# Optimization experiments

Hardware: AMD Instinct MI355X
Metric: run time of the kernel (lower is better)

## Reference

```python
import jax, jax.numpy as jnp
import numpy as np

E = 262144   # num edges
T = 1048576  # num triplets
H = 128      # hidden_channels
IE = 64      # int_emb_size
NR = 6       # num_radial
NS = 7       # num_spherical
BD = 8       # basis_emb_size_dist
BA = 8       # basis_emb_size_angle


def setup_inputs() -> dict:
    key = jax.random.key(0)
    ks = jax.random.split(key, 32)
    def rnd(k, shape, s=0.1):
        return jax.random.normal(k, shape, dtype=jnp.float32) * s
    return {
        "x1": rnd(ks[0], (T, H), 1.0),
        "x_old": rnd(ks[1], (E, H), 1.0),
        "rbf0": rnd(ks[2], (E, NR), 1.0),
        "sbf": rnd(ks[3], (T, NS * NR), 1.0),
        "idx_kj": jax.random.randint(ks[4], (T,), 0, E),
        "idx_ji": jax.random.randint(ks[5], (T,), 0, E),
        "W_rbf1": rnd(ks[6], (NR, BD)),
        "W_rbf2": rnd(ks[7], (BD, H)),
        "W_sbf1": rnd(ks[8], (NS * NR, BA)),
        "W_sbf2": rnd(ks[9], (BA, IE)),
        "W_rbf": rnd(ks[10], (NR, H)),
        "W_kj": rnd(ks[11], (H, H)), "b_kj": rnd(ks[12], (H,)),
        "W_ji": rnd(ks[13], (H, H)), "b_ji": rnd(ks[14], (H,)),
        "W_connect": rnd(ks[15], (H, H)), "b_connect": rnd(ks[16], (H,)),
        "W_get_up": rnd(ks[17], (H, H)), "b_get_up": rnd(ks[18], (H,)),
        "W_down": rnd(ks[19], (H, IE)), "b_down": rnd(ks[20], (IE,)),
        "W_up": rnd(ks[21], (IE, H)), "b_up": rnd(ks[22], (H,)),
        "res_before_W": rnd(ks[23], (1, 2, H, H)), "res_before_b": rnd(ks[24], (1, 2, H)),
        "W_lin": rnd(ks[25], (H, H)), "b_lin": rnd(ks[26], (H,)),
        "res_after_W": rnd(ks[27], (2, 2, H, H)), "res_after_b": rnd(ks[28], (2, 2, H)),
    }


def _residual(x, W, b):
    # x + act(lin2(act(lin1(x))))
    h = jax.nn.silu(x @ W[0] + b[0])
    return x + jax.nn.silu(h @ W[1] + b[1])


def reference(x1, x_old, rbf0, sbf, idx_kj, idx_ji, W_rbf1, W_rbf2, W_sbf1, W_sbf2,
              W_rbf, W_kj, b_kj, W_ji, b_ji, W_connect, b_connect, W_get_up, b_get_up,
              W_down, b_down, W_up, b_up, res_before_W, res_before_b, W_lin, b_lin,
              res_after_W, res_after_b):
    act = jax.nn.silu  # swish
    nE = x_old.shape[0]
    # aggregate plane features onto edges
    x_up = jax.ops.segment_sum(x1, idx_ji, num_segments=nE)
    x_up = act(x_up @ W_get_up + b_get_up)
    x_ji = act(x_old @ W_ji + b_ji)
    x_kj = act(x_old @ W_kj + b_kj)
    rbf = (rbf0 @ W_rbf1) @ W_rbf2            # [E, H]
    x_kj = x_kj * rbf
    x_kj = act(x_kj @ W_down + b_down)        # [E, IE]
    sbf_p = (sbf @ W_sbf1) @ W_sbf2           # [T, IE]
    x_kj = x_kj[idx_kj] * sbf_p               # gather edges -> triplets
    x_kj = jax.ops.segment_sum(x_kj, idx_ji, num_segments=nE)  # scatter back to edges
    x_kj = act(x_kj @ W_up + b_up)
    e1 = x_ji + x_kj
    e1 = act(e1 @ W_connect + b_connect) + x_up
    for i in range(res_before_W.shape[0]):
        e1 = _residual(e1, res_before_W[i], res_before_b[i])
    e1 = act(e1 @ W_lin + b_lin) + x_old
    for i in range(res_after_W.shape[0]):
        e1 = _residual(e1, res_after_W[i], res_after_b[i])
    e2 = (rbf0 @ W_rbf) * e1
    return (e1, e2)
```

## Files before the change

### kernel.cpp

```cpp
#include <hip/hip_runtime.h>

#define E_N 262144
#define T_N 1048576

typedef short  bf16x8  __attribute__((ext_vector_type(8)));
typedef short  bf16x4v __attribute__((ext_vector_type(4)));
typedef float  f32x4   __attribute__((ext_vector_type(4)));

#define OFF_KJ    0
#define OFF_DOWN  16384
#define OFF_UP    24576
#define OFF_JI    32768
#define OFF_GU    49152
#define OFF_CN    65536
#define OFF_RB0   81920
#define OFF_RB1   98304
#define OFF_LIN   114688
#define OFF_RA00  131072
#define OFF_RA01  147456
#define OFF_RA10  163840
#define OFF_RA11  180224
#define OFF_END   196608
#define WREG_BYTES 524288u

#define OFFB_AGG   0u
#define OFFB_XKJ   33554432u
#define OFFB_WREG  67108864u
#define OFFB_CNT   67633152u
#define OFFB_POS   68683776u
#define OFFB_TRI   69732352u
#define OFFB_BS    73926656u
#define OFFB_BP    73927680u

__device__ __forceinline__ float silu_f(float x) { return x / (1.0f + __expf(-x)); }

__device__ __forceinline__ unsigned short f2bf(float f) {
  union { float f; unsigned int u; } v; v.f = f;
  unsigned int u = v.u;
  return (unsigned short)((u + 0x7fffu + ((u >> 16) & 1u)) >> 16);
}
__device__ __forceinline__ float bf2f(unsigned short h) {
  union { unsigned int u; float f; } v; v.u = ((unsigned int)h) << 16;
  return v.f;
}

__device__ __forceinline__ unsigned cvtpk(float lo, float hi) {
  unsigned r;
  asm("v_cvt_pk_bf16_f32 %0, %1, %2" : "=v"(r) : "v"(lo), "v"(hi));
  return r;
}

template<int NC, int NR, int NTH>
__device__ __forceinline__ void stage_tile(const float* __restrict__ g, char* __restrict__ lds) {
  constexpr int RB = NC * 2;
  constexpr int C4 = NC / 4;
  for (int i = threadIdx.x; i < NR * C4; i += NTH) {
    int r = i / C4, c4 = i % C4;
    float4 v = *(const float4*)(g + (size_t)r * NC + c4 * 4);
    bf16x4v h;
    h[0] = (short)f2bf(v.x); h[1] = (short)f2bf(v.y);
    h[2] = (short)f2bf(v.z); h[3] = (short)f2bf(v.w);
    *(bf16x4v*)(lds + r * RB + ((c4 * 8) ^ ((r & 7) << 4))) = h;
  }
}

__device__ __forceinline__ void stage_tile_bf16_64(const unsigned short* __restrict__ g,
                                                   char* __restrict__ lds) {
  int i = threadIdx.x;
  int r = i >> 3, c = i & 7;
  int4 v = *(const int4*)((const char*)g + r * 128 + c * 16);
  *(int4*)(lds + r * 128 + ((c * 16) ^ ((r & 7) << 4))) = v;
}

template<int MREP, int NREP, int KSTEPS, int RB>
__device__ __forceinline__ void mfma_gemm(const char* __restrict__ lds, int row0, int col0,
                                          const unsigned short* __restrict__ WT, int lane,
                                          f32x4 (&acc)[MREP][NREP]) {
  const int kg = lane >> 4, r15 = lane & 15;
#pragma unroll
  for (int m = 0; m < MREP; ++m)
#pragma unroll
    for (int n = 0; n < NREP; ++n) acc[m][n] = (f32x4){0.f, 0.f, 0.f, 0.f};
#pragma unroll
  for (int kk = 0; kk < KSTEPS; ++kk) {
    bf16x8 a[MREP], bfr[NREP];
#pragma unroll
    for (int m = 0; m < MREP; ++m) {
      int row = row0 + m * 16 + r15;
      a[m] = *(const bf16x8*)(lds + row * RB + ((kk * 64 + kg * 16) ^ ((row & 7) << 4)));
    }
#pragma unroll
    for (int n = 0; n < NREP; ++n) {
      int nc = col0 + n * 16 + r15;
      bfr[n] = *(const bf16x8*)((const short*)WT + nc * (KSTEPS * 32) + kk * 32 + kg * 8);
    }
#pragma unroll
    for (int m = 0; m < MREP; ++m)
#pragma unroll
      for (int n = 0; n < NREP; ++n)
        acc[m][n] = __builtin_amdgcn_mfma_f32_16x16x32_bf16(a[m], bfr[n], acc[m][n], 0, 0, 0);
  }
}

template<int RB>
__device__ __forceinline__ void write_cd(char* __restrict__ lds, int wrow, int wcol, int lane,
                                         const f32x4 (&v)[2][2]) {
  const int kg = lane >> 4, r15 = lane & 15;
#pragma unroll
  for (int m = 0; m < 2; ++m)
#pragma unroll
    for (int n = 0; n < 2; ++n) {
      int col2 = (wcol + n * 16 + r15) * 2;
      int row0 = wrow + m * 16 + kg * 4;
      unsigned u0 = cvtpk(v[m][n][0], v[m][n][1]);
      unsigned u1 = cvtpk(v[m][n][2], v[m][n][3]);
      *(unsigned short*)(lds + (row0 + 0) * RB + (col2 ^ (((row0 + 0) & 7) << 4))) = (unsigned short)u0;
      *(unsigned short*)(lds + (row0 + 1) * RB + (col2 ^ (((row0 + 1) & 7) << 4))) = (unsigned short)(u0 >> 16);
      *(unsigned short*)(lds + (row0 + 2) * RB + (col2 ^ (((row0 + 2) & 7) << 4))) = (unsigned short)u1;
      *(unsigned short*)(lds + (row0 + 3) * RB + (col2 ^ (((row0 + 3) & 7) << 4))) = (unsigned short)(u1 >> 16);
    }
}

__global__ void __launch_bounds__(256) k_prep(
    const float* __restrict__ W_kj, const float* __restrict__ W_down,
    const float* __restrict__ W_up, const float* __restrict__ W_ji,
    const float* __restrict__ W_get_up, const float* __restrict__ W_connect,
    const float* __restrict__ rbW, const float* __restrict__ W_lin,
    const float* __restrict__ raW,
    const float* __restrict__ W_rbf1, const float* __restrict__ W_rbf2,
    unsigned short* __restrict__ wreg) {
  int b = blockIdx.x;
  if (b == 13) {
    float* W12 = (float*)(wreg + OFF_END);
    for (int i = threadIdx.x; i < 768; i += 256) {
      int r = i >> 7, n = i & 127;
      float s = 0.f;
#pragma unroll
      for (int q = 0; q < 8; ++q) s += W_rbf1[r * 8 + q] * W_rbf2[q * 128 + n];
      W12[i] = s;
    }
    return;
  }
  const float* src; int K = 128, N = 128; int off;
  switch (b) {
    case 0:  src = W_kj;          off = OFF_KJ;  break;
    case 1:  src = W_down;        off = OFF_DOWN; N = 64;  break;
    case 2:  src = W_up;          off = OFF_UP;   K = 64;  break;
    case 3:  src = W_ji;          off = OFF_JI;  break;
    case 4:  src = W_get_up;      off = OFF_GU;  break;
    case 5:  src = W_connect;     off = OFF_CN;  break;
    case 6:  src = rbW;           off = OFF_RB0; break;
    case 7:  src = rbW + 16384;   off = OFF_RB1; break;
    case 8:  src = W_lin;         off = OFF_LIN; break;
    case 9:  src = raW;           off = OFF_RA00; break;
    case 10: src = raW + 16384;   off = OFF_RA01; break;
    case 11: src = raW + 32768;   off = OFF_RA10; break;
    default: src = raW + 49152;   off = OFF_RA11; break;
  }
  unsigned short* dst = wreg + off;
  for (int i = threadIdx.x; i < K * N; i += 256) {
    int k = i / N, n = i % N;
    dst[n * K + k] = f2bf(src[i]);
  }
}

__global__ void __launch_bounds__(256) k_hist(const int* __restrict__ idx_ji,
                                              int* __restrict__ counts) {
  int t = blockIdx.x * 256 + threadIdx.x;
  atomicAdd(&counts[idx_ji[t]], 1);
}

__global__ void __launch_bounds__(1024) k_scan1(const int* __restrict__ counts,
                                                int* __restrict__ locpre,
                                                int* __restrict__ bsum) {
  __shared__ int s[1024];
  int i = blockIdx.x * 1024 + threadIdx.x;
  int v = counts[i];
  s[threadIdx.x] = v; __syncthreads();
  for (int o = 1; o < 1024; o <<= 1) {
    int t = (threadIdx.x >= o) ? s[threadIdx.x - o] : 0;
    __syncthreads();
    s[threadIdx.x] += t;
    __syncthreads();
  }
  locpre[i] = s[threadIdx.x] - v;
  if (threadIdx.x == 1023) bsum[blockIdx.x] = s[1023];
}

__global__ void __launch_bounds__(256) k_scan2(const int* __restrict__ bsum,
                                               int* __restrict__ bpre, int* __restrict__ offs) {
  __shared__ int s[256];
  int v = bsum[threadIdx.x];
  s[threadIdx.x] = v; __syncthreads();
  for (int o = 1; o < 256; o <<= 1) {
    int t = (threadIdx.x >= o) ? s[threadIdx.x - o] : 0;
    __syncthreads();
    s[threadIdx.x] += t;
    __syncthreads();
  }
  bpre[threadIdx.x] = s[threadIdx.x] - v;
  if (threadIdx.x == 0) offs[E_N] = T_N;
}

__global__ void __launch_bounds__(1024) k_scan3(const int* __restrict__ locpre,
                                                const int* __restrict__ bpre,
                                                int* __restrict__ offs,
                                                int* __restrict__ pos) {
  int i = blockIdx.x * 1024 + threadIdx.x;
  int v = locpre[i] + bpre[blockIdx.x];
  offs[i] = v;
  pos[i] = v;
}

__global__ void __launch_bounds__(256) k_fill(const int* __restrict__ idx_ji,
                                              int* __restrict__ pos, int* __restrict__ tri) {
  int t = blockIdx.x * 256 + threadIdx.x;
  int e = idx_ji[t];
  int slot = atomicAdd(&pos[e], 1);
  tri[slot] = t;
}

__global__ void __launch_bounds__(256) k_sbfp(const float* __restrict__ sbf,
                                              const float* __restrict__ W_sbf1,
                                              const float* __restrict__ W_sbf2,
                                              unsigned int* __restrict__ sbfp) {
  __shared__ float s_s[8][42];
  __shared__ float s_t8[8][8];
  int t0 = blockIdx.x * 8;
  for (int i = threadIdx.x; i < 8 * 42; i += 256)
    s_s[i / 42][i % 42] = sbf[(size_t)t0 * 42 + i];
  __syncthreads();
  if (threadIdx.x < 64) {
    int w8 = threadIdx.x >> 3, bb = threadIdx.x & 7;
    float s = 0.f;
#pragma unroll
    for (int r = 0; r < 42; ++r) s += s_s[w8][r] * W_sbf1[r * 8 + bb];
    s_t8[w8][bb] = s;
  }
  __syncthreads();
  int w8 = threadIdx.x >> 5, jj = threadIdx.x & 31;
  float sp0 = 0.f, sp1 = 0.f;
#pragma unroll
  for (int bb = 0; bb < 8; ++bb) {
    float tv = s_t8[w8][bb];
    sp0 += tv * W_sbf2[bb * 64 + jj * 2];
    sp1 += tv * W_sbf2[bb * 64 + jj * 2 + 1];
  }
  unsigned int u = (unsigned int)f2bf(sp0) | ((unsigned int)f2bf(sp1) << 16);
  sbfp[(size_t)(t0 + w8) * 32 + jj] = u;
}

__global__ void __launch_bounds__(256) k_aggB(const int* __restrict__ offs,
                                              const int* __restrict__ tri,
                                              const int* __restrict__ idx_kj,
                                              const unsigned int* __restrict__ sbfp,
                                              const unsigned int* __restrict__ xkj,
                                              unsigned int* __restrict__ agg) {
  int sub = threadIdx.x >> 5, jj = threadIdx.x & 31;
  int e = blockIdx.x * 8 + sub;
  int o0 = offs[e], o1 = offs[e + 1];
  float a0 = 0.f, a1 = 0.f;
  for (int i = o0; i < o1; ++i) {
    int t = tri[i];
    int kj = idx_kj[t];
    unsigned int sv = sbfp[(size_t)t * 32 + jj];
    unsigned int xv = xkj[(size_t)kj * 32 + jj];
    a0 += bf2f((unsigned short)(sv & 0xffff)) * bf2f((unsigned short)(xv & 0xffff));
    a1 += bf2f((unsigned short)(sv >> 16)) * bf2f((unsigned short)(xv >> 16));
  }
  agg[(size_t)e * 32 + jj] = (unsigned int)f2bf(a0) | ((unsigned int)f2bf(a1) << 16);
}

__global__ void __launch_bounds__(256) k_xupg(const int* __restrict__ offs,
                                              const int* __restrict__ tri,
                                              const float* __restrict__ x1,
                                              float* __restrict__ out) {
  int sub = threadIdx.x >> 6, h2 = threadIdx.x & 63;
  int e = blockIdx.x * 4 + sub;
  int o0 = offs[e], o1 = offs[e + 1];
  float a0 = 0.f, a1 = 0.f;
  for (int i = o0; i < o1; ++i) {
    int t = tri[i];
    float2 v = *(const float2*)(x1 + (size_t)t * 128 + h2 * 2);
    a0 += v.x; a1 += v.y;
  }
  *(float2*)(out + (size_t)e * 128 + h2 * 2) = make_float2(a0, a1);
}

__global__ void __launch_bounds__(512, 4) phaseA(
    const float* __restrict__ x_old, const float* __restrict__ rbf0,
    const unsigned short* __restrict__ wreg,
    const float* __restrict__ b_kj, const float* __restrict__ b_down,
    unsigned short* __restrict__ xkjdown) {
  __shared__ char lds[32768];
  char* B0 = lds;
  char* B1 = lds + 16384;
  const int tid = threadIdx.x, lane = tid & 63, wave = tid >> 6;
  const int kg = lane >> 4, r15 = lane & 15;
  const int wrow = (wave >> 2) * 32, wcol = (wave & 3) * 32;
  const size_t e_base = (size_t)blockIdx.x * 64;
  const float* W12 = (const float*)(wreg + OFF_END);

  stage_tile<128, 64, 512>(x_old + e_base * 128, B0);
  __syncthreads();

  f32x4 acc[2][2], val[2][2];
  mfma_gemm<2, 2, 4, 256>(B0, wrow, wcol, wreg + OFF_KJ, lane, acc);
#pragma unroll
  for (int n = 0; n < 2; ++n) {
    int col = wcol + n * 16 + r15;
    float bk = b_kj[col];
    float wc[6];
#pragma unroll
    for (int q = 0; q < 6; ++q) wc[q] = W12[q * 128 + col];
#pragma unroll
    for (int m = 0; m < 2; ++m)
#pragma unroll
      for (int r = 0; r < 4; ++r) {
        int row = wrow + m * 16 + kg * 4 + r;
        const float* rp = rbf0 + (e_base + row) * 6;
        float rv = rp[0]*wc[0] + rp[1]*wc[1] + rp[2]*wc[2] + rp[3]*wc[3] + rp[4]*wc[4] + rp[5]*wc[5];
        val[m][n][r] = silu_f(acc[m][n][r] + bk) * rv;
      }
  }
  write_cd<256>(B1, wrow, wcol, lane, val);
  __syncthreads();

  const int wrow2 = (wave >> 1) * 16, wcol2 = (wave & 1) * 32;
  f32x4 a2[1][2];
  mfma_gemm<1, 2, 4, 256>(B1, wrow2, wcol2, wreg + OFF_DOWN, lane, a2);
#pragma unroll
  for (int n = 0; n < 2; ++n) {
    int col = wcol2 + n * 16 + r15;
    float bd = b_down[col];
#pragma unroll
    for (int r = 0; r < 4; ++r) {
      int row = wrow2 + kg * 4 + r;
      xkjdown[(e_base + row) * 64 + col] = f2bf(silu_f(a2[0][n][r] + bd));
    }
  }
}

__global__ void __launch_bounds__(512, 4) phaseC1(
    const float* __restrict__ x_old, float* __restrict__ e1buf,
    const unsigned short* __restrict__ agg, const unsigned short* __restrict__ wreg,
    const float* __restrict__ b_up, const float* __restrict__ b_ji,
    const float* __restrict__ b_get_up, const float* __restrict__ b_connect,
    const float* __restrict__ rbB, const float* __restrict__ b_lin,
    const float* __restrict__ raB,
    const float* __restrict__ rbf0, const float* __restrict__ W_rbf,
    float* __restrict__ e2o) {
  __shared__ char lds[73728];
  char* X0   = lds;
  char* X1   = lds + 16384;
  char* X2   = lds + 32768;
  char* XOLD = lds + 49152;
  char* AGGB = lds + 65536;
  const int tid = threadIdx.x, lane = tid & 63, wave = tid >> 6;
  const int kg = lane >> 4, r15 = lane & 15;
  const int wrow = (wave >> 2) * 32, wcol = (wave & 3) * 32;
  const size_t e_base = (size_t)blockIdx.x * 64;

  stage_tile<128, 64, 512>(x_old + e_base * 128, XOLD);
  stage_tile<128, 64, 512>(e1buf + e_base * 128, X1);
  stage_tile_bf16_64(agg + e_base * 64, AGGB);
  __syncthreads();

  f32x4 acc[2][2], keep[2][2], h[2][2];

  mfma_gemm<2, 2, 2, 128>(AGGB, wrow, wcol, wreg + OFF_UP, lane, acc);
#pragma unroll
  for (int n = 0; n < 2; ++n) {
    float bu = b_up[wcol + n * 16 + r15];
#pragma unroll
    for (int m = 0; m < 2; ++m)
#pragma unroll
      for (int r = 0; r < 4; ++r) h[m][n][r] = silu_f(acc[m][n][r] + bu);
  }
  mfma_gemm<2, 2, 4, 256>(XOLD, wrow, wcol, wreg + OFF_JI, lane, acc);
#pragma unroll
  for (int n = 0; n < 2; ++n) {
    float bj = b_ji[wcol + n * 16 + r15];
#pragma unroll
    for (int m = 0; m < 2; ++m)
#pragma unroll
      for (int r = 0; r < 4; ++r) keep[m][n][r] = silu_f(acc[m][n][r] + bj) + h[m][n][r];
  }
  write_cd<256>(X0, wrow, wcol, lane, keep);
  __syncthreads();

  mfma_gemm<2, 2, 4, 256>(X1, wrow, wcol, wreg + OFF_GU, lane, acc);
#pragma unroll
  for (int n = 0; n < 2; ++n) {
    float bg = b_get_up[wcol + n * 16 + r15];
#pragma unroll
    for (int m = 0; m < 2; ++m)
#pragma unroll
      for (int r = 0; r < 4; ++r) h[m][n][r] = silu_f(acc[m][n][r] + bg);
  }
  mfma_gemm<2, 2, 4, 256>(X0, wrow, wcol, wreg + OFF_CN, lane, acc);
#pragma unroll
  for (int n = 0; n < 2; ++n) {
    float bc = b_connect[wcol + n * 16 + r15];
#pragma unroll
    for (int m = 0; m < 2; ++m)
#pragma unroll
      for (int r = 0; r < 4; ++r) keep[m][n][r] = silu_f(acc[m][n][r] + bc) + h[m][n][r];
  }
  write_cd<256>(X2, wrow, wcol, lane, keep);
  __syncthreads();

  mfma_gemm<2, 2, 4, 256>(X2, wrow, wcol, wreg + OFF_RB0, lane, acc);
#pragma unroll
  for (int n = 0; n < 2; ++n) {
    float bv = rbB[wcol + n * 16 + r15];
#pragma unroll
    for (int m = 0; m < 2; ++m)
#pragma unroll
      for (int r = 0; r < 4; ++r) h[m][n][r] = silu_f(acc[m][n][r] + bv);
  }
  write_cd<256>(X0, wrow, wcol, lane, h);
  __syncthreads();

  mfma_gemm<2, 2, 4, 256>(X0, wrow, wcol, wreg + OFF_RB1, lane, acc);
#pragma unroll
  for (int n = 0; n < 2; ++n) {
    float bv = rbB[128 + wcol + n * 16 + r15];
#pragma unroll
    for (int m = 0; m < 2; ++m)
#pragma unroll
      for (int r = 0; r < 4; ++r) keep[m][n][r] += silu_f(acc[m][n][r] + bv);
  }
  write_cd<256>(X1, wrow, wcol, lane, keep);
  __syncthreads();

  mfma_gemm<2, 2, 4, 256>(X1, wrow, wcol, wreg + OFF_LIN, lane, acc);
#pragma unroll
  for (int n = 0; n < 2; ++n) {
    int col = wcol + n * 16 + r15;
    float bl = b_lin[col];
#pragma unroll
    for (int m = 0; m < 2; ++m)
#pragma unroll
      for (int r = 0; r < 4; ++r) {
        int row = wrow + m * 16 + kg * 4 + r;
        float xo = bf2f(*(const unsigned short*)(XOLD + row * 256 + ((col * 2) ^ ((row & 7) << 4))));
        keep[m][n][r] = silu_f(acc[m][n][r] + bl) + xo;
      }
  }
  write_cd<256>(X2, wrow, wcol, lane, keep);
  __syncthreads();

  mfma_gemm<2, 2, 4, 256>(X2, wrow, wcol, wreg + OFF_RA00, lane, acc);
#pragma unroll
  for (int n = 0; n < 2; ++n) {
    float bv = raB[wcol + n * 16 + r15];
#pragma unroll
    for (int m = 0; m < 2; ++m)
#pragma unroll
      for (int r = 0; r < 4; ++r) h[m][n][r] = silu_f(acc[m][n][r] + bv);
  }
  write_cd<256>(X0, wrow, wcol, lane, h);
  __syncthreads();

  mfma_gemm<2, 2, 4, 256>(X0, wrow, wcol, wreg + OFF_RA01, lane, acc);
#pragma unroll
  for (int n = 0; n < 2; ++n) {
    float bv = raB[128 + wcol + n * 16 + r15];
#pragma unroll
    for (int m = 0; m < 2; ++m)
#pragma unroll
      for (int r = 0; r < 4; ++r) keep[m][n][r] += silu_f(acc[m][n][r] + bv);
  }
  write_cd<256>(X1, wrow, wcol, lane, keep);
  __syncthreads();

  mfma_gemm<2, 2, 4, 256>(X1, wrow, wcol, wreg + OFF_RA10, lane, acc);
#pragma unroll
  for (int n = 0; n < 2; ++n) {
    float bv = raB[256 + wcol + n * 16 + r15];
#pragma unroll
    for (int m = 0; m < 2; ++m)
#pragma unroll
      for (int r = 0; r < 4; ++r) h[m][n][r] = silu_f(acc[m][n][r] + bv);
  }
  write_cd<256>(X2, wrow, wcol, lane, h);
  __syncthreads();

  mfma_gemm<2, 2, 4, 256>(X2, wrow, wcol, wreg + OFF_RA11, lane, acc);
#pragma unroll
  for (int n = 0; n < 2; ++n) {
    int col = wcol + n * 16 + r15;
    float bv = raB[384 + col];
    float wc[6];
#pragma unroll
    for (int q = 0; q < 6; ++q) wc[q] = W_rbf[q * 128 + col];
#pragma unroll
    for (int m = 0; m < 2; ++m)
#pragma unroll
      for (int r = 0; r < 4; ++r) {
        int row = wrow + m * 16 + kg * 4 + r;
        size_t e = e_base + row;
        float val = keep[m][n][r] + silu_f(acc[m][n][r] + bv);
        e1buf[e * 128 + col] = val;
        if (e2o) {
          const float* rp = rbf0 + e * 6;
          float rv = rp[0]*wc[0] + rp[1]*wc[1] + rp[2]*wc[2] + rp[3]*wc[3] + rp[4]*wc[4] + rp[5]*wc[5];
          e2o[e * 128 + col] = val * rv;
        }
      }
  }
}

__global__ void __launch_bounds__(256) k_e2(const float* __restrict__ e1,
                                            const float* __restrict__ rbf0,
                                            const float* __restrict__ W_rbf,
                                            float* __restrict__ e2) {
  size_t gid = (size_t)blockIdx.x * 256 + threadIdx.x;
  int e = (int)(gid >> 5);
  int c = (int)(gid & 31) << 2;
  float r6[6];
#pragma unroll
  for (int r = 0; r < 6; ++r) r6[r] = rbf0[(size_t)e * 6 + r];
  float4 v = *(const float4*)(e1 + (size_t)e * 128 + c);
  float4 o;
  float rv;
  rv = 0.f;
#pragma unroll
  for (int r = 0; r < 6; ++r) rv += r6[r] * W_rbf[r * 128 + c + 0];
  o.x = v.x * rv;
  rv = 0.f;
#pragma unroll
  for (int r = 0; r < 6; ++r) rv += r6[r] * W_rbf[r * 128 + c + 1];
  o.y = v.y * rv;
  rv = 0.f;
#pragma unroll
  for (int r = 0; r < 6; ++r) rv += r6[r] * W_rbf[r * 128 + c + 2];
  o.z = v.z * rv;
  rv = 0.f;
#pragma unroll
  for (int r = 0; r < 6; ++r) rv += r6[r] * W_rbf[r * 128 + c + 3];
  o.w = v.w * rv;
  *(float4*)(e2 + (size_t)e * 128 + c) = o;
}

extern "C" void kernel_launch(void* const* d_in, const int* in_sizes, int n_in,
                              void* d_out, int out_size, void* d_ws, size_t ws_size,
                              hipStream_t stream) {
  const float* x1        = (const float*)d_in[0];
  const float* x_old     = (const float*)d_in[1];
  const float* rbf0      = (const float*)d_in[2];
  const float* sbf       = (const float*)d_in[3];
  const int*   idx_kj    = (const int*)d_in[4];
  const int*   idx_ji    = (const int*)d_in[5];
  const float* W_rbf1    = (const float*)d_in[6];
  const float* W_rbf2    = (const float*)d_in[7];
  const float* W_sbf1    = (const float*)d_in[8];
  const float* W_sbf2    = (const float*)d_in[9];
  const float* W_rbf     = (const float*)d_in[10];
  const float* W_kj      = (const float*)d_in[11];
  const float* b_kj      = (const float*)d_in[12];
  const float* W_ji      = (const float*)d_in[13];
  const float* b_ji      = (const float*)d_in[14];
  const float* W_connect = (const float*)d_in[15];
  const float* b_connect = (const float*)d_in[16];
  const float* W_get_up  = (const float*)d_in[17];
  const float* b_get_up  = (const float*)d_in[18];
  const float* W_down    = (const float*)d_in[19];
  const float* b_down    = (const float*)d_in[20];
  const float* W_up      = (const float*)d_in[21];
  const float* b_up      = (const float*)d_in[22];
  const float* rbW       = (const float*)d_in[23];
  const float* rbB       = (const float*)d_in[24];
  const float* W_lin     = (const float*)d_in[25];
  const float* b_lin     = (const float*)d_in[26];
  const float* raW       = (const float*)d_in[27];
  const float* raB       = (const float*)d_in[28];

  float* e1buf = (float*)d_out;
  char*  base2 = (char*)d_out + (size_t)E_N * 128 * 4;
  float* e2out = (float*)base2;

  unsigned short* xkj_b = (unsigned short*)(base2 + OFFB_XKJ);
  int* counts = (int*)(base2 + OFFB_CNT);
  int* pos    = (int*)(base2 + OFFB_POS);
  int* tri    = (int*)(base2 + OFFB_TRI);
  int* bsum   = (int*)(base2 + OFFB_BS);
  int* bpre   = (int*)(base2 + OFFB_BP);

  const size_t need_ws = (size_t)WREG_BYTES + (size_t)E_N * 64 * 2;
  const bool fuse = ws_size >= need_ws;
  unsigned short* wreg  = fuse ? (unsigned short*)d_ws
                               : (unsigned short*)(base2 + OFFB_WREG);
  unsigned short* agg_b = fuse ? (unsigned short*)((char*)d_ws + WREG_BYTES)
                               : (unsigned short*)(base2 + OFFB_AGG);

  unsigned int* sbfp_u = (unsigned int*)e1buf;

  k_prep<<<14, 256, 0, stream>>>(W_kj, W_down, W_up, W_ji, W_get_up, W_connect,
                                 rbW, W_lin, raW, W_rbf1, W_rbf2, wreg);

  hipMemsetAsync(counts, 0, (E_N + 1) * sizeof(int), stream);
  k_hist<<<T_N / 256, 256, 0, stream>>>(idx_ji, counts);
  k_scan1<<<256, 1024, 0, stream>>>(counts, pos, bsum);
  k_scan2<<<1, 256, 0, stream>>>(bsum, bpre, counts);
  k_scan3<<<256, 1024, 0, stream>>>(pos, bpre, counts, pos);
  k_fill<<<T_N / 256, 256, 0, stream>>>(idx_ji, pos, tri);

  k_sbfp<<<T_N / 8, 256, 0, stream>>>(sbf, W_sbf1, W_sbf2, sbfp_u);

  phaseA<<<E_N / 64, 512, 0, stream>>>(x_old, rbf0, wreg, b_kj, b_down, xkj_b);

  k_aggB<<<E_N / 8, 256, 0, stream>>>(counts, tri, idx_kj, sbfp_u,
                                      (const unsigned int*)xkj_b, (unsigned int*)agg_b);

  k_xupg<<<E_N / 4, 256, 0, stream>>>(counts, tri, x1, e1buf);

  phaseC1<<<E_N / 64, 512, 0, stream>>>(x_old, e1buf, agg_b, wreg,
                                        b_up, b_ji, b_get_up, b_connect, rbB, b_lin, raB,
                                        rbf0, W_rbf, fuse ? e2out : nullptr);
  if (!fuse)
    k_e2<<<E_N * 32 / 256, 256, 0, stream>>>(e1buf, rbf0, W_rbf, e2out);
}
```

Baseline: 1.348 ms.

## Shrink phaseC1 LDS footprint, read agg and x_old residual from global, add setprio

phaseC1's LDS allocation drops from 72KB to 48KB. The agg tile is no longer staged; its A fragments are read straight from global memory. The x_old residual in the W_lin epilogue is now read in fp32 from global instead of the bf16 LDS copy, which lets x_old be staged into the X2 buffer. The launch-bounds occupancy hint rises from 4 to 6 blocks to use the freed LDS. The change also adds s_setprio around the MFMA loops and uses packed v_cvt_pk_bf16 conversions. The risks are higher register pressure under the tighter bound and extra global traffic for agg and x_old.

```diff
diff --git a/kernel.cpp b/kernel.cpp
--- a/kernel.cpp
+++ b/kernel.cpp
@@ -4,7 +4,6 @@
 #define T_N 1048576
 
 typedef short  bf16x8  __attribute__((ext_vector_type(8)));
-typedef short  bf16x4v __attribute__((ext_vector_type(4)));
 typedef float  f32x4   __attribute__((ext_vector_type(4)));
 
 #define OFF_KJ    0
@@ -57,19 +56,11 @@
   for (int i = threadIdx.x; i < NR * C4; i += NTH) {
     int r = i / C4, c4 = i % C4;
     float4 v = *(const float4*)(g + (size_t)r * NC + c4 * 4);
-    bf16x4v h;
-    h[0] = (short)f2bf(v.x); h[1] = (short)f2bf(v.y);
-    h[2] = (short)f2bf(v.z); h[3] = (short)f2bf(v.w);
-    *(bf16x4v*)(lds + r * RB + ((c4 * 8) ^ ((r & 7) << 4))) = h;
-  }
-}
-
-__device__ __forceinline__ void stage_tile_bf16_64(const unsigned short* __restrict__ g,
-                                                   char* __restrict__ lds) {
-  int i = threadIdx.x;
-  int r = i >> 3, c = i & 7;
-  int4 v = *(const int4*)((const char*)g + r * 128 + c * 16);
-  *(int4*)(lds + r * 128 + ((c * 16) ^ ((r & 7) << 4))) = v;
+    uint2 u;
+    u.x = cvtpk(v.x, v.y);
+    u.y = cvtpk(v.z, v.w);
+    *(uint2*)(lds + r * RB + ((c4 * 8) ^ ((r & 7) << 4))) = u;
+  }
 }
 
 template<int MREP, int NREP, int KSTEPS, int RB>
@@ -81,6 +72,7 @@
   for (int m = 0; m < MREP; ++m)
 #pragma unroll
     for (int n = 0; n < NREP; ++n) acc[m][n] = (f32x4){0.f, 0.f, 0.f, 0.f};
+  __builtin_amdgcn_s_setprio(1);
 #pragma unroll
   for (int kk = 0; kk < KSTEPS; ++kk) {
     bf16x8 a[MREP], bfr[NREP];
@@ -100,6 +92,38 @@
       for (int n = 0; n < NREP; ++n)
         acc[m][n] = __builtin_amdgcn_mfma_f32_16x16x32_bf16(a[m], bfr[n], acc[m][n], 0, 0, 0);
   }
+  __builtin_amdgcn_s_setprio(0);
+}
+
+template<int MREP, int NREP, int KSTEPS, int RS>
+__device__ __forceinline__ void mfma_gemm_gA(const unsigned short* __restrict__ gA,
+                                             int row0, int col0,
+                                             const unsigned short* __restrict__ WT, int lane,
+                                             f32x4 (&acc)[MREP][NREP]) {
+  const int kg = lane >> 4, r15 = lane & 15;
+#pragma unroll
+  for (int m = 0; m < MREP; ++m)
+#pragma unroll
+    for (int n = 0; n < NREP; ++n) acc[m][n] = (f32x4){0.f, 0.f, 0.f, 0.f};
+  __builtin_amdgcn_s_setprio(1);
+#pragma unroll
+  for (int kk = 0; kk < KSTEPS; ++kk) {
+    bf16x8 a[MREP], bfr[NREP];
+#pragma unroll
+    for (int m = 0; m < MREP; ++m)
+      a[m] = *(const bf16x8*)(gA + (size_t)(row0 + m * 16 + r15) * RS + kk * 32 + kg * 8);
+#pragma unroll
+    for (int n = 0; n < NREP; ++n) {
+      int nc = col0 + n * 16 + r15;
+      bfr[n] = *(const bf16x8*)((const short*)WT + nc * (KSTEPS * 32) + kk * 32 + kg * 8);
+    }
+#pragma unroll
+    for (int m = 0; m < MREP; ++m)
+#pragma unroll
+      for (int n = 0; n < NREP; ++n)
+        acc[m][n] = __builtin_amdgcn_mfma_f32_16x16x32_bf16(a[m], bfr[n], acc[m][n], 0, 0, 0);
+  }
+  __builtin_amdgcn_s_setprio(0);
 }
 
 template<int RB>
@@ -246,8 +270,7 @@
     sp0 += tv * W_sbf2[bb * 64 + jj * 2];
     sp1 += tv * W_sbf2[bb * 64 + jj * 2 + 1];
   }
-  unsigned int u = (unsigned int)f2bf(sp0) | ((unsigned int)f2bf(sp1) << 16);
-  sbfp[(size_t)(t0 + w8) * 32 + jj] = u;
+  sbfp[(size_t)(t0 + w8) * 32 + jj] = cvtpk(sp0, sp1);
 }
 
 __global__ void __launch_bounds__(256) k_aggB(const int* __restrict__ offs,
@@ -268,7 +291,7 @@
     a0 += bf2f((unsigned short)(sv & 0xffff)) * bf2f((unsigned short)(xv & 0xffff));
     a1 += bf2f((unsigned short)(sv >> 16)) * bf2f((unsigned short)(xv >> 16));
   }
-  agg[(size_t)e * 32 + jj] = (unsigned int)f2bf(a0) | ((unsigned int)f2bf(a1) << 16);
+  agg[(size_t)e * 32 + jj] = cvtpk(a0, a1);
 }
 
 __global__ void __launch_bounds__(256) k_xupg(const int* __restrict__ offs,
@@ -341,7 +364,7 @@
   }
 }
 
-__global__ void __launch_bounds__(512, 4) phaseC1(
+__global__ void __launch_bounds__(512, 6) phaseC1(
     const float* __restrict__ x_old, float* __restrict__ e1buf,
     const unsigned short* __restrict__ agg, const unsigned short* __restrict__ wreg,
     const float* __restrict__ b_up, const float* __restrict__ b_ji,
@@ -350,25 +373,22 @@
     const float* __restrict__ raB,
     const float* __restrict__ rbf0, const float* __restrict__ W_rbf,
     float* __restrict__ e2o) {
-  __shared__ char lds[73728];
-  char* X0   = lds;
-  char* X1   = lds + 16384;
-  char* X2   = lds + 32768;
-  char* XOLD = lds + 49152;
-  char* AGGB = lds + 65536;
+  __shared__ char lds[49152];
+  char* X0 = lds;
+  char* X1 = lds + 16384;
+  char* X2 = lds + 32768;
   const int tid = threadIdx.x, lane = tid & 63, wave = tid >> 6;
   const int kg = lane >> 4, r15 = lane & 15;
   const int wrow = (wave >> 2) * 32, wcol = (wave & 3) * 32;
   const size_t e_base = (size_t)blockIdx.x * 64;
 
-  stage_tile<128, 64, 512>(x_old + e_base * 128, XOLD);
+  stage_tile<128, 64, 512>(x_old + e_base * 128, X2);
   stage_tile<128, 64, 512>(e1buf + e_base * 128, X1);
-  stage_tile_bf16_64(agg + e_base * 64, AGGB);
   __syncthreads();
 
   f32x4 acc[2][2], keep[2][2], h[2][2];
 
-  mfma_gemm<2, 2, 2, 128>(AGGB, wrow, wcol, wreg + OFF_UP, lane, acc);
+  mfma_gemm_gA<2, 2, 2, 64>(agg + e_base * 64, wrow, wcol, wreg + OFF_UP, lane, acc);
 #pragma unroll
   for (int n = 0; n < 2; ++n) {
     float bu = b_up[wcol + n * 16 + r15];
@@ -377,7 +397,7 @@
 #pragma unroll
       for (int r = 0; r < 4; ++r) h[m][n][r] = silu_f(acc[m][n][r] + bu);
   }
-  mfma_gemm<2, 2, 4, 256>(XOLD, wrow, wcol, wreg + OFF_JI, lane, acc);
+  mfma_gemm<2, 2, 4, 256>(X2, wrow, wcol, wreg + OFF_JI, lane, acc);
 #pragma unroll
   for (int n = 0; n < 2; ++n) {
     float bj = b_ji[wcol + n * 16 + r15];
@@ -444,8 +464,7 @@
 #pragma unroll
       for (int r = 0; r < 4; ++r) {
         int row = wrow + m * 16 + kg * 4 + r;
-        float xo = bf2f(*(const unsigned short*)(XOLD + row * 256 + ((col * 2) ^ ((row & 7) << 4))));
-        keep[m][n][r] = silu_f(acc[m][n][r] + bl) + xo;
+        keep[m][n][r] = silu_f(acc[m][n][r] + bl) + x_old[(e_base + row) * 128 + col];
       }
   }
   write_cd<256>(X2, wrow, wcol, lane, keep);
```

After: 1.446 ms. 7.3% more time.
